# Kernel optimization log

Hardware: AMD Instinct MI355X
Metric: run time of the kernel (lower is better)

The kernel has to match this reference:

```python
import jax, jax.numpy as jnp
import numpy as np

CHUNK = 8          # n in original code
TRIU_K = 1         # k in original code
ALPHA = 0.1        # config.alpha
_IU = np.triu_indices(CHUNK, k=TRIU_K)  # 28 upper-triangular pairs per 8x8 chunk


def setup_inputs() -> dict:
    key = jax.random.key(0)
    k1, k2, k3 = jax.random.split(key, 3)
    B, T, C = 128, 1024, 64
    N, D = B * T, 512
    y_pred_logits = jax.random.normal(k1, (N, C), dtype=jnp.float32)
    y_feat = jax.random.normal(k2, (N, D), dtype=jnp.float32)
    y_true = jax.random.normal(k3, (B, T, C), dtype=jnp.float32)
    return {"y_pred_logits": y_pred_logits, "y_feat": y_feat, "y_true": y_true}


def reference(y_pred_logits, y_feat, y_true):
    N, D = y_feat.shape
    # --- chunked pairwise cosine similarity, vectorized over all 8-row chunks ---
    chunks = y_feat.reshape(N // CHUNK, CHUNK, D)             # [nc, 8, D]
    dot = jnp.einsum('cid,cjd->cij', chunks, chunks)          # [nc, 8, 8]
    norms = jnp.sqrt(jnp.einsum('cii->ci', dot))              # [nc, 8]
    sim = dot / (norms[:, None, :] * norms[:, :, None])       # [nc, 8, 8]
    feat_dist_loss = (1.0 - sim[:, _IU[0], _IU[1]]).sum()     # sum over all chunks/pairs
    # --- MSE loss (reduction='mean') ---
    B, T, C = y_true.shape
    targets = y_true.reshape(B * T, C)
    mse = jnp.mean((y_pred_logits - targets) ** 2)
    return mse + ALPHA * feat_dist_loss
```

## Files before the change

kernel.cpp:

```cpp
#include <hip/hip_runtime.h>

#define NC          8388608
#define NCHUNK      16384
#define ALPHA       0.1f
#define FEAT_BLOCKS 2048
#define MSE_BLOCKS  512
#define TOTAL_BLOCKS (FEAT_BLOCKS + MSE_BLOCKS)

template<int ctrl, int rmask>
__device__ __forceinline__ float dpp_add(float v) {
    int t = __builtin_amdgcn_update_dpp(0, __float_as_int(v), ctrl, rmask, 0xf, true);
    return v + __int_as_float(t);
}

__device__ __forceinline__ float wave_reduce_dpp(float v) {
    v = dpp_add<0xB1,  0xf>(v);
    v = dpp_add<0x4E,  0xf>(v);
    v = dpp_add<0x141, 0xf>(v);
    v = dpp_add<0x140, 0xf>(v);
    v = dpp_add<0x142, 0xa>(v);
    v = dpp_add<0x143, 0xc>(v);
    return v;
}

__global__ __launch_bounds__(256) void fused_kernel(const float* __restrict__ feat,
                                                    const float* __restrict__ pred,
                                                    const float* __restrict__ tgt,
                                                    float* __restrict__ part) {
    const int lane = threadIdx.x & 63;
    const int wave = threadIdx.x >> 6;
    __shared__ float bsum[4];

    if (blockIdx.x < FEAT_BLOCKS) {
        const int wid = blockIdx.x * 4 + wave;
        float wacc = 0.f;
        for (int chunk = wid; chunk < NCHUNK; chunk += FEAT_BLOCKS * 4) {
            const float4* base = (const float4*)(feat + (size_t)chunk * 8 * 512);
            float a[8][8];
            #pragma unroll
            for (int i = 0; i < 8; ++i) {
                float4 v1 = base[i * 128 + lane];
                float4 v2 = base[i * 128 + 64 + lane];
                a[i][0] = v1.x; a[i][1] = v1.y; a[i][2] = v1.z; a[i][3] = v1.w;
                a[i][4] = v2.x; a[i][5] = v2.y; a[i][6] = v2.z; a[i][7] = v2.w;
            }

            float p[36];
            #pragma unroll
            for (int i = 0; i < 8; ++i) {
                #pragma unroll
                for (int j = i; j < 8; ++j) {
                    const int idx = 8 * i - (i * (i - 1)) / 2 + (j - i);
                    float s = 0.f;
                    #pragma unroll
                    for (int k = 0; k < 8; ++k) s = fmaf(a[i][k], a[j][k], s);
                    p[idx] = s;
                }
            }

            #pragma unroll
            for (int k = 0; k < 36; ++k) p[k] = wave_reduce_dpp(p[k]);

            if (lane == 63) {
                const int diag[8] = {0, 8, 15, 21, 26, 30, 33, 35};
                float rn[8];
                #pragma unroll
                for (int i = 0; i < 8; ++i) rn[i] = rsqrtf(p[diag[i]]);
                float acc = 0.f;
                #pragma unroll
                for (int i = 0; i < 8; ++i) {
                    #pragma unroll
                    for (int j = i + 1; j < 8; ++j) {
                        const int idx = 8 * i - (i * (i - 1)) / 2 + (j - i);
                        acc = fmaf(p[idx], rn[i] * rn[j], acc);
                    }
                }
                wacc += 28.0f - acc;
            }
        }
        if (lane == 63) bsum[wave] = wacc;
        __syncthreads();
        if (threadIdx.x == 0)
            part[blockIdx.x] = ALPHA * ((bsum[0] + bsum[1]) + (bsum[2] + bsum[3]));
    } else {
        const int bid = blockIdx.x - FEAT_BLOCKS;
        const float4* p4 = (const float4*)pred;
        const float4* t4 = (const float4*)tgt;
        const int n4 = NC / 4;
        float s = 0.f;
        for (int i = bid * blockDim.x + threadIdx.x; i < n4;
             i += MSE_BLOCKS * blockDim.x) {
            float4 a = p4[i], b = t4[i];
            float dx = a.x - b.x, dy = a.y - b.y, dz = a.z - b.z, dw = a.w - b.w;
            s += dx * dx + dy * dy + dz * dz + dw * dw;
        }
        s = wave_reduce_dpp(s);
        if (lane == 63) bsum[wave] = s;
        __syncthreads();
        if (threadIdx.x == 0)
            part[blockIdx.x] = ((bsum[0] + bsum[1]) + (bsum[2] + bsum[3]))
                               * (1.0f / (float)NC);
    }
}

__global__ __launch_bounds__(256) void final_reduce(const float* __restrict__ part,
                                                    float* __restrict__ out) {
    const int lane = threadIdx.x & 63;
    const int wave = threadIdx.x >> 6;
    float s = 0.f;
    #pragma unroll
    for (int r = 0; r < TOTAL_BLOCKS / 256; ++r)
        s += part[r * 256 + threadIdx.x];
    s = wave_reduce_dpp(s);
    __shared__ float bsum[4];
    if (lane == 63) bsum[wave] = s;
    __syncthreads();
    if (threadIdx.x == 0)
        out[0] = (bsum[0] + bsum[1]) + (bsum[2] + bsum[3]);
}

extern "C" void kernel_launch(void* const* d_in, const int* in_sizes, int n_in,
                              void* d_out, int out_size, void* d_ws, size_t ws_size,
                              hipStream_t stream) {
    const float* y_pred = (const float*)d_in[0];
    const float* y_feat = (const float*)d_in[1];
    const float* y_true = (const float*)d_in[2];
    float* out = (float*)d_out;
    float* ws  = (float*)d_ws;

    fused_kernel<<<TOTAL_BLOCKS, 256, 0, stream>>>(y_feat, y_pred, y_true, ws);
    final_reduce<<<1, 256, 0, stream>>>(ws, out);
}
```

Baseline: 59.74 us.

## Merge MSE and feature work into every block with fully unrolled fixed trip counts

Instead of splitting blocks into separate feature-similarity and MSE roles, every block now does four float4 MSE elements per thread plus two feature chunks per wave, with both loops fully unrolled to constant trip counts. The two partial sums are combined per wave before one shared block reduction, and the grid shrinks to 2048 blocks. The aim is to balance memory traffic evenly across blocks and expose more independent loads per thread, removing the imbalance between heterogeneous block types. Trip counts are now hardcoded to the exact problem size, and each thread's register pressure rises.

```diff
diff --git a/kernel.cpp b/kernel.cpp
--- a/kernel.cpp
+++ b/kernel.cpp
@@ -1,11 +1,9 @@
 #include <hip/hip_runtime.h>
 
-#define NC          8388608
-#define NCHUNK      16384
-#define ALPHA       0.1f
-#define FEAT_BLOCKS 2048
-#define MSE_BLOCKS  512
-#define TOTAL_BLOCKS (FEAT_BLOCKS + MSE_BLOCKS)
+#define NC       8388608
+#define NCHUNK   16384
+#define ALPHA    0.1f
+#define NBLOCKS  2048
 
 template<int ctrl, int rmask>
 __device__ __forceinline__ float dpp_add(float v) {
@@ -31,76 +29,72 @@
     const int wave = threadIdx.x >> 6;
     __shared__ float bsum[4];
 
-    if (blockIdx.x < FEAT_BLOCKS) {
-        const int wid = blockIdx.x * 4 + wave;
-        float wacc = 0.f;
-        for (int chunk = wid; chunk < NCHUNK; chunk += FEAT_BLOCKS * 4) {
-            const float4* base = (const float4*)(feat + (size_t)chunk * 8 * 512);
-            float a[8][8];
+    const float4* p4 = (const float4*)pred;
+    const float4* t4 = (const float4*)tgt;
+    float ms = 0.f;
+    #pragma unroll
+    for (int k = 0; k < 4; ++k) {
+        const int i = (k * NBLOCKS + blockIdx.x) * 256 + threadIdx.x;
+        float4 a = p4[i], b = t4[i];
+        float dx = a.x - b.x, dy = a.y - b.y, dz = a.z - b.z, dw = a.w - b.w;
+        ms += dx * dx + dy * dy + dz * dz + dw * dw;
+    }
+
+    const int wid = blockIdx.x * 4 + wave;
+    float wacc = 0.f;
+    #pragma unroll
+    for (int s = 0; s < 2; ++s) {
+        const int chunk = wid + s * (NBLOCKS * 4);
+        const float4* base = (const float4*)(feat + (size_t)chunk * 8 * 512);
+        float a[8][8];
+        #pragma unroll
+        for (int i = 0; i < 8; ++i) {
+            float4 v1 = base[i * 128 + lane];
+            float4 v2 = base[i * 128 + 64 + lane];
+            a[i][0] = v1.x; a[i][1] = v1.y; a[i][2] = v1.z; a[i][3] = v1.w;
+            a[i][4] = v2.x; a[i][5] = v2.y; a[i][6] = v2.z; a[i][7] = v2.w;
+        }
+
+        float p[36];
+        #pragma unroll
+        for (int i = 0; i < 8; ++i) {
             #pragma unroll
-            for (int i = 0; i < 8; ++i) {
-                float4 v1 = base[i * 128 + lane];
-                float4 v2 = base[i * 128 + 64 + lane];
-                a[i][0] = v1.x; a[i][1] = v1.y; a[i][2] = v1.z; a[i][3] = v1.w;
-                a[i][4] = v2.x; a[i][5] = v2.y; a[i][6] = v2.z; a[i][7] = v2.w;
+            for (int j = i; j < 8; ++j) {
+                const int idx = 8 * i - (i * (i - 1)) / 2 + (j - i);
+                float s2 = 0.f;
+                #pragma unroll
+                for (int k = 0; k < 8; ++k) s2 = fmaf(a[i][k], a[j][k], s2);
+                p[idx] = s2;
             }
+        }
 
-            float p[36];
+        #pragma unroll
+        for (int k = 0; k < 36; ++k) p[k] = wave_reduce_dpp(p[k]);
+
+        if (lane == 63) {
+            const int diag[8] = {0, 8, 15, 21, 26, 30, 33, 35};
+            float rn[8];
+            #pragma unroll
+            for (int i = 0; i < 8; ++i) rn[i] = rsqrtf(p[diag[i]]);
+            float acc = 0.f;
             #pragma unroll
             for (int i = 0; i < 8; ++i) {
                 #pragma unroll
-                for (int j = i; j < 8; ++j) {
+                for (int j = i + 1; j < 8; ++j) {
                     const int idx = 8 * i - (i * (i - 1)) / 2 + (j - i);
-                    float s = 0.f;
-                    #pragma unroll
-                    for (int k = 0; k < 8; ++k) s = fmaf(a[i][k], a[j][k], s);
-                    p[idx] = s;
+                    acc = fmaf(p[idx], rn[i] * rn[j], acc);
                 }
             }
+            wacc += 28.0f - acc;
+        }
+    }
 
-            #pragma unroll
-            for (int k = 0; k < 36; ++k) p[k] = wave_reduce_dpp(p[k]);
-
-            if (lane == 63) {
-                const int diag[8] = {0, 8, 15, 21, 26, 30, 33, 35};
-                float rn[8];
-                #pragma unroll
-                for (int i = 0; i < 8; ++i) rn[i] = rsqrtf(p[diag[i]]);
-                float acc = 0.f;
-                #pragma unroll
-                for (int i = 0; i < 8; ++i) {
-                    #pragma unroll
-                    for (int j = i + 1; j < 8; ++j) {
-                        const int idx = 8 * i - (i * (i - 1)) / 2 + (j - i);
-                        acc = fmaf(p[idx], rn[i] * rn[j], acc);
-                    }
-                }
-                wacc += 28.0f - acc;
-            }
-        }
-        if (lane == 63) bsum[wave] = wacc;
-        __syncthreads();
-        if (threadIdx.x == 0)
-            part[blockIdx.x] = ALPHA * ((bsum[0] + bsum[1]) + (bsum[2] + bsum[3]));
-    } else {
-        const int bid = blockIdx.x - FEAT_BLOCKS;
-        const float4* p4 = (const float4*)pred;
-        const float4* t4 = (const float4*)tgt;
-        const int n4 = NC / 4;
-        float s = 0.f;
-        for (int i = bid * blockDim.x + threadIdx.x; i < n4;
-             i += MSE_BLOCKS * blockDim.x) {
-            float4 a = p4[i], b = t4[i];
-            float dx = a.x - b.x, dy = a.y - b.y, dz = a.z - b.z, dw = a.w - b.w;
-            s += dx * dx + dy * dy + dz * dz + dw * dw;
-        }
-        s = wave_reduce_dpp(s);
-        if (lane == 63) bsum[wave] = s;
-        __syncthreads();
-        if (threadIdx.x == 0)
-            part[blockIdx.x] = ((bsum[0] + bsum[1]) + (bsum[2] + bsum[3]))
-                               * (1.0f / (float)NC);
-    }
+    ms = wave_reduce_dpp(ms);
+    if (lane == 63)
+        bsum[wave] = ALPHA * wacc + ms * (1.0f / (float)NC);
+    __syncthreads();
+    if (threadIdx.x == 0)
+        part[blockIdx.x] = (bsum[0] + bsum[1]) + (bsum[2] + bsum[3]);
 }
 
 __global__ __launch_bounds__(256) void final_reduce(const float* __restrict__ part,
@@ -109,7 +103,7 @@
     const int wave = threadIdx.x >> 6;
     float s = 0.f;
     #pragma unroll
-    for (int r = 0; r < TOTAL_BLOCKS / 256; ++r)
+    for (int r = 0; r < NBLOCKS / 256; ++r)
         s += part[r * 256 + threadIdx.x];
     s = wave_reduce_dpp(s);
     __shared__ float bsum[4];
@@ -128,6 +122,6 @@
     float* out = (float*)d_out;
     float* ws  = (float*)d_ws;
 
-    fused_kernel<<<TOTAL_BLOCKS, 256, 0, stream>>>(y_feat, y_pred, y_true, ws);
+    fused_kernel<<<NBLOCKS, 256, 0, stream>>>(y_feat, y_pred, y_true, ws);
     final_reduce<<<1, 256, 0, stream>>>(ws, out);
 }
```

New measurement: 62.97 us. +5.4%, slower.
